# Kernel optimization log

Measured on AMD Instinct MI355X. Metric: run time of the kernel, lower is better.

The kernel has to match this reference:

```python
import jax, jax.numpy as jnp
import numpy as np
from jax import lax

B, C, H, W = 32, 192, 56, 56
HEADS = 8
HD = C // HEADS
SCALE = HD ** -0.5
EPS = 1e-5


def _ln(t, g, b):
    m = jnp.mean(t, axis=-1, keepdims=True)
    v = jnp.mean((t - m) ** 2, axis=-1, keepdims=True)
    return (t - m) / jnp.sqrt(v + EPS) * g + b


def setup_inputs() -> dict:
    ks = jax.random.split(jax.random.key(0), 8)
    x = jax.random.normal(ks[0], (B, C, H, W), jnp.float32)
    bn_gamma = jnp.ones((C,), jnp.float32)
    bn_beta = jnp.zeros((C,), jnp.float32)
    bn_mean = jax.random.normal(ks[1], (C,), jnp.float32) * 0.1
    bn_var = jax.random.uniform(ks[2], (C,), jnp.float32) + 0.5
    conv_w = jax.random.normal(ks[3], (C, 1, 7, 7), jnp.float32) * 0.02  # depthwise, groups=C
    conv_b = jnp.zeros((C,), jnp.float32)
    qkv_w = jax.random.normal(ks[4], (3 * C, C), jnp.float32) * 0.02
    qkv_b = jnp.zeros((3 * C,), jnp.float32)
    ln0_g = jnp.ones((C,), jnp.float32); ln0_b = jnp.zeros((C,), jnp.float32)
    ln1_g = jnp.ones((C,), jnp.float32); ln1_b = jnp.zeros((C,), jnp.float32)
    return {"x": x, "bn_gamma": bn_gamma, "bn_beta": bn_beta, "bn_mean": bn_mean,
            "bn_var": bn_var, "conv_w": conv_w, "conv_b": conv_b,
            "qkv_w": qkv_w, "qkv_b": qkv_b,
            "ln0_g": ln0_g, "ln0_b": ln0_b, "ln1_g": ln1_g, "ln1_b": ln1_b}


def reference(x, bn_gamma, bn_beta, bn_mean, bn_var, conv_w, conv_b,
              qkv_w, qkv_b, ln0_g, ln0_b, ln1_g, ln1_b):
    Bx, Cx, Hx, Wx = x.shape
    N = Hx * Wx
    Bw = Bx * N // 4  # number of 2x2 windows

    # --- window partition: [B,C,H,W] -> [B*N/4, 4, C]
    windows = x.reshape(Bx, Cx, Hx // 2, 2, Wx // 2, 2)
    windows = windows.transpose(0, 2, 4, 3, 5, 1).reshape(Bw, 4, Cx)

    # --- guide-token generator: BN(inference) -> GELU -> depthwise 7x7 s2 conv
    xb = (x - bn_mean[:, None, None]) / jnp.sqrt(bn_var[:, None, None] + EPS)
    xb = xb * bn_gamma[:, None, None] + bn_beta[:, None, None]
    xg = jax.nn.gelu(xb, approximate=False)
    g = lax.conv_general_dilated(xg, conv_w, window_strides=(2, 2),
                                 padding=[(3, 3), (3, 3)],
                                 feature_group_count=Cx,
                                 dimension_numbers=("NCHW", "OIHW", "NCHW"))
    g = g + conv_b[None, :, None, None]              # [B,C,H/2,W/2]
    guide = g.reshape(Bx, Cx, N // 4).transpose(0, 2, 1).reshape(Bw, 1, Cx)

    # --- 5-token windows: guide + 4 local tokens
    tok = jnp.concatenate([guide, windows], axis=1)  # [Bw,5,C]
    t = _ln(tok, ln0_g, ln0_b)

    # --- tiny attention over 5 tokens
    qkv = t @ qkv_w.T + qkv_b                        # [Bw,5,3C]
    qkv = qkv.reshape(Bw, 5, 3, HEADS, HD).transpose(2, 0, 3, 1, 4)  # [3,Bw,h,5,hd]
    q, k, v = qkv[0], qkv[1], qkv[2]
    attn = jax.nn.softmax(jnp.einsum("bhqd,bhkd->bhqk", q, k) * SCALE, axis=-1)
    o = jnp.einsum("bhqk,bhkd->bhqd", attn, v)       # [Bw,h,5,hd]
    o = o.transpose(0, 2, 1, 3).reshape(Bw, 5, Cx)

    out = o[:, 0].reshape(Bx, Hx // 2, Wx // 2, Cx)
    return _ln(out, ln1_g, ln1_b)
```

## Files before the change

### kernel.cpp

```cpp
#include <hip/hip_runtime.h>
#include <hip/hip_bf16.h>
#include <cmath>

#define B_    32
#define C_    192
#define H_    56
#define W_    56
#define EPS_  1e-5f
#define SCALE_ 0.20412414523193154f

using bf = __hip_bfloat16;
typedef __attribute__((ext_vector_type(8))) short short8;
typedef __attribute__((ext_vector_type(4))) float f32x4;

__global__ void k_wconv(const float* __restrict__ qkv_w, bf* __restrict__ wbf) {
    int i = blockIdx.x * 256 + threadIdx.x;
    if (i < 576 * 192) wbf[i] = __float2bfloat16(qkv_w[i]);
}

__global__ __launch_bounds__(256) void k_act_ptok(
        const float* __restrict__ x,
        const float* __restrict__ ln0g, const float* __restrict__ ln0b,
        bf* __restrict__ ptok) {
    __shared__ float tile[C_ * 57];
    __shared__ float mv[W_], rv[W_];
    int b = blockIdx.x / H_, h = blockIdx.x % H_;
    const size_t xbase = ((size_t)b * C_ * H_ + h) * W_;

    for (int f = threadIdx.x; f < C_ * W_; f += 256) {
        int c = f / W_, w = f % W_;
        tile[c * 57 + w] = x[xbase + (size_t)c * (H_ * W_) + w];
    }
    __syncthreads();
    if (threadIdx.x < 224) {
        int p = threadIdx.x >> 2, q = threadIdx.x & 3;
        float S = 0.f, Q = 0.f;
        #pragma unroll 8
        for (int j = 0; j < 48; j++) {
            float v = tile[(q * 48 + j) * 57 + p];
            S += v; Q += v * v;
        }
        S += __shfl_xor(S, 1); Q += __shfl_xor(Q, 1);
        S += __shfl_xor(S, 2); Q += __shfl_xor(Q, 2);
        if (q == 0) {
            float mean = S * (1.f / 192.f);
            float var  = Q * (1.f / 192.f) - mean * mean;
            mv[p] = mean; rv[p] = rsqrtf(var + EPS_);
        }
    }
    __syncthreads();
    const size_t pbase = (((size_t)b * H_ + h) * W_) * C_;
    for (int f = threadIdx.x; f < W_ * C_; f += 256) {
        int p = f / C_, c = f % C_;
        float v = (tile[c * 57 + p] - mv[p]) * rv[p] * ln0g[c] + ln0b[c];
        ptok[pbase + (size_t)p * C_ + c] = __float2bfloat16(v);
    }
}

__global__ __launch_bounds__(256) void k_conv(
        const float* __restrict__ x,
        const float* __restrict__ bn_g, const float* __restrict__ bn_b,
        const float* __restrict__ bn_m, const float* __restrict__ bn_v,
        const float* __restrict__ cw, const float* __restrict__ cb,
        float* __restrict__ gbuf) {
    __shared__ float pl[62 * 63];
    int tid = threadIdx.x;
    int bc = blockIdx.x;
    int c = bc % C_;

    for (int i = tid; i < 62 * 63; i += 256) pl[i] = 0.f;
    __syncthreads();

    float bm = bn_m[c];
    float rs = rsqrtf(bn_v[c] + EPS_) * bn_g[c];
    float bb = bn_b[c];
    const float* xp = x + (size_t)bc * (H_ * W_);
    for (int i = tid; i < 784; i += 256) {
        int row = i / 14, j = i % 14;
        float4 v = *(const float4*)(xp + row * W_ + j * 4);
        float* dst = &pl[(row + 3) * 63 + j * 4 + 3];
        #pragma unroll
        for (int e = 0; e < 4; e++) {
            float xv = (e == 0) ? v.x : (e == 1) ? v.y : (e == 2) ? v.z : v.w;
            float xn = (xv - bm) * rs + bb;
            dst[e] = 0.5f * xn * (1.0f + erff(xn * 0.70710678118654752f));
        }
    }
    __syncthreads();

    float wr[49];
    #pragma unroll
    for (int i = 0; i < 49; i++) wr[i] = cw[c * 49 + i];
    float cbv = cb[c];

    for (int o = tid; o < 784; o += 256) {
        int oh = o / 28, ow = o % 28;
        const float* base = &pl[(2 * oh) * 63 + 2 * ow];
        float acc = cbv;
        #pragma unroll
        for (int kh = 0; kh < 7; kh++) {
            #pragma unroll
            for (int kw = 0; kw < 7; kw++)
                acc += wr[kh * 7 + kw] * base[kh * 63 + kw];
        }
        gbuf[(size_t)bc * 784 + o] = acc;
    }
}

__global__ __launch_bounds__(256) void k_gtok(
        const float* __restrict__ gbuf,
        const float* __restrict__ ln0g, const float* __restrict__ ln0b,
        bf* __restrict__ gtok) {
    __shared__ float tile[C_ * 29];
    __shared__ float mv[28], rv[28];
    int b = blockIdx.x / 28, oh = blockIdx.x % 28;
    size_t gbase = ((size_t)b * C_ * 784) + (size_t)oh * 28;
    for (int f = threadIdx.x; f < C_ * 28; f += 256) {
        int c = f / 28, w = f % 28;
        tile[c * 29 + w] = gbuf[gbase + (size_t)c * 784 + w];
    }
    __syncthreads();
    if (threadIdx.x < 112) {
        int p = threadIdx.x >> 2, q = threadIdx.x & 3;
        float S = 0.f, Q = 0.f;
        #pragma unroll 8
        for (int j = 0; j < 48; j++) {
            float v = tile[(q * 48 + j) * 29 + p];
            S += v; Q += v * v;
        }
        S += __shfl_xor(S, 1); Q += __shfl_xor(Q, 1);
        S += __shfl_xor(S, 2); Q += __shfl_xor(Q, 2);
        if (q == 0) {
            float mean = S * (1.f / 192.f);
            float var  = Q * (1.f / 192.f) - mean * mean;
            mv[p] = mean; rv[p] = rsqrtf(var + EPS_);
        }
    }
    __syncthreads();
    size_t tbase = ((size_t)b * 784 + (size_t)oh * 28) * C_;
    for (int f = threadIdx.x; f < 28 * C_; f += 256) {
        int p = f / C_, c = f % C_;
        float v = (tile[c * 29 + p] - mv[p]) * rv[p] * ln0g[c] + ln0b[c];
        gtok[tbase + (size_t)p * C_ + c] = __float2bfloat16(v);
    }
}

template<int COLOFS>
__global__ __launch_bounds__(256) void k_gemm(
        const bf* __restrict__ A, const bf* __restrict__ wbf,
        const float* __restrict__ qkv_b, bf* __restrict__ out) {
    __shared__ unsigned char Asm_[128 * 384];
    int tid = threadIdx.x;
    size_t r0 = (size_t)blockIdx.x * 128;

    for (int i = tid; i < 128 * 24; i += 256) {
        int row = i / 24, j = i % 24;
        uint4 v = *(const uint4*)((const unsigned char*)(A + (r0 + row) * C_) + j * 16);
        *(uint4*)(Asm_ + row * 384 + ((j * 16) ^ ((row & 7) << 4))) = v;
    }
    __syncthreads();

    int wid = tid >> 6, lane = tid & 63, lo = lane & 15, hi = lane >> 4;
    int xorv = (lo & 7) << 4;
    constexpr int NT = (576 - COLOFS) / 16;
    constexpr int OUTW = 576 - COLOFS;
    for (int nt = wid; nt < NT; nt += 4) {
        int col = COLOFS + nt * 16 + lo;
        float bias = qkv_b[col];
        f32x4 acc[8];
        #pragma unroll
        for (int m = 0; m < 8; m++) acc[m] = {bias, bias, bias, bias};
        const unsigned char* bbase = (const unsigned char*)wbf + (size_t)col * 384 + hi * 16;
        #pragma unroll
        for (int ks = 0; ks < 6; ks++) {
            short8 bfrag = *(const short8*)(bbase + ks * 64);
            int kb = (ks * 64 + hi * 16) ^ xorv;
            #pragma unroll
            for (int m = 0; m < 8; m++) {
                short8 a = *(const short8*)(Asm_ + (m * 16 + lo) * 384 + kb);
                acc[m] = __builtin_amdgcn_mfma_f32_16x16x32_bf16(a, bfrag, acc[m], 0, 0, 0);
            }
        }
        #pragma unroll
        for (int m = 0; m < 8; m++) {
            #pragma unroll
            for (int r = 0; r < 4; r++) {
                int row = m * 16 + hi * 4 + r;
                out[(r0 + row) * OUTW + (col - COLOFS)] = __float2bfloat16(acc[m][r]);
            }
        }
    }
}

__global__ __launch_bounds__(256) void k_att2(
        const bf* __restrict__ kvp, const bf* __restrict__ qkvg,
        const float* __restrict__ ln1g, const float* __restrict__ ln1b,
        float* __restrict__ out) {
    int tg = blockIdx.x * 256 + threadIdx.x;
    int bw = tg >> 3, hh = tg & 7;
    int b = bw / 784, rr = bw % 784;
    int oh = rr / 28, ow = rr % 28;

    const bf* qb = qkvg + (size_t)bw * 576 + hh * 24;
    float q[24];
    #pragma unroll
    for (int j = 0; j < 3; j++) {
        short8 v = *(const short8*)(qb + j * 8);
        #pragma unroll
        for (int e = 0; e < 8; e++)
            q[j * 8 + e] = __uint_as_float(((unsigned)(unsigned short)v[e]) << 16);
    }
    size_t pr[4];
    #pragma unroll
    for (int t = 0; t < 4; t++) {
        int h = 2 * oh + (t >> 1), w = 2 * ow + (t & 1);
        pr[t] = ((size_t)b * H_ + h) * W_ + w;
    }

    float s[5];
    {
        float a = 0.f;
        #pragma unroll
        for (int j = 0; j < 3; j++) {
            short8 v = *(const short8*)(qb + 192 + j * 8);
            #pragma unroll
            for (int e = 0; e < 8; e++)
                a += q[j * 8 + e] * __uint_as_float(((unsigned)(unsigned short)v[e]) << 16);
        }
        s[0] = a * SCALE_;
    }
    #pragma unroll
    for (int t = 0; t < 4; t++) {
        const bf* kb = kvp + pr[t] * 384 + hh * 24;
        float a = 0.f;
        #pragma unroll
        for (int j = 0; j < 3; j++) {
            short8 v = *(const short8*)(kb + j * 8);
            #pragma unroll
            for (int e = 0; e < 8; e++)
                a += q[j * 8 + e] * __uint_as_float(((unsigned)(unsigned short)v[e]) << 16);
        }
        s[t + 1] = a * SCALE_;
    }
    float mx = fmaxf(fmaxf(fmaxf(s[0], s[1]), fmaxf(s[2], s[3])), s[4]);
    float sum = 0.f;
    #pragma unroll
    for (int t = 0; t < 5; t++) { s[t] = expf(s[t] - mx); sum += s[t]; }
    float inv = 1.f / sum;
    #pragma unroll
    for (int t = 0; t < 5; t++) s[t] *= inv;

    float o[24];
    #pragma unroll
    for (int d = 0; d < 24; d++) o[d] = 0.f;
    {
        #pragma unroll
        for (int j = 0; j < 3; j++) {
            short8 v = *(const short8*)(qb + 384 + j * 8);
            #pragma unroll
            for (int e = 0; e < 8; e++)
                o[j * 8 + e] += s[0] * __uint_as_float(((unsigned)(unsigned short)v[e]) << 16);
        }
    }
    #pragma unroll
    for (int t = 0; t < 4; t++) {
        const bf* vb = kvp + pr[t] * 384 + 192 + hh * 24;
        #pragma unroll
        for (int j = 0; j < 3; j++) {
            short8 v = *(const short8*)(vb + j * 8);
            #pragma unroll
            for (int e = 0; e < 8; e++)
                o[j * 8 + e] += s[t + 1] * __uint_as_float(((unsigned)(unsigned short)v[e]) << 16);
        }
    }

    float S = 0.f, Q = 0.f;
    #pragma unroll
    for (int d = 0; d < 24; d++) { S += o[d]; Q += o[d] * o[d]; }
    S += __shfl_xor(S, 1); Q += __shfl_xor(Q, 1);
    S += __shfl_xor(S, 2); Q += __shfl_xor(Q, 2);
    S += __shfl_xor(S, 4); Q += __shfl_xor(Q, 4);
    float mean = S * (1.f / 192.f);
    float var  = Q * (1.f / 192.f) - mean * mean;
    float rstd = rsqrtf(var + EPS_);
    float* ob = out + (size_t)bw * 192 + hh * 24;
    #pragma unroll
    for (int d = 0; d < 24; d++)
        ob[d] = (o[d] - mean) * rstd * ln1g[hh * 24 + d] + ln1b[hh * 24 + d];
}

__global__ __launch_bounds__(256) void k_attn(
        const bf* __restrict__ gtok, const bf* __restrict__ ptok,
        const bf* __restrict__ wbf, const float* __restrict__ qkv_b,
        const float* __restrict__ ln1g, const float* __restrict__ ln1b,
        float* __restrict__ out) {
    __shared__ unsigned char Asm_[48 * 384];
    __shared__ bf q0s[8][192];
    __shared__ bf kvs[2][5][8][192];
    int tid = threadIdx.x;
    int wb0 = blockIdx.x * 8;

    for (int idx = tid; idx < 48 * 24; idx += 256) {
        int row = idx / 24, j = idx % 24;
        int t = row >> 3, win = row & 7;
        uint4 val = {0u, 0u, 0u, 0u};
        if (t < 5) {
            const unsigned char* src;
            if (t == 0) {
                src = (const unsigned char*)(gtok + (size_t)(wb0 + win) * C_) + j * 16;
            } else {
                int bw = wb0 + win;
                int b = bw / 784; int rr = bw - b * 784;
                int oh = rr / 28, ow = rr - oh * 28;
                int h = 2 * oh + ((t - 1) >> 1), w = 2 * ow + ((t - 1) & 1);
                src = (const unsigned char*)(ptok + (((size_t)b * H_ + h) * W_ + w) * C_) + j * 16;
            }
            val = *(const uint4*)src;
        }
        *(uint4*)(Asm_ + row * 384 + ((j * 16) ^ ((row & 7) << 4))) = val;
    }
    __syncthreads();

    int wid = tid >> 6, lane = tid & 63, lo = lane & 15, hi = lane >> 4;
    int xorv = (lo & 7) << 4;
    for (int nn = 0; nn < 9; nn++) {
        int nt = nn * 4 + wid;
        int col = nt * 16 + lo;
        int mtop = (nt < 12) ? 1 : 3;
        float bias = qkv_b[col];
        f32x4 acc0 = {bias, bias, bias, bias};
        f32x4 acc1 = acc0, acc2 = acc0;
        const unsigned char* bbase = (const unsigned char*)wbf + (size_t)col * 384 + hi * 16;
        #pragma unroll
        for (int ks = 0; ks < 6; ks++) {
            short8 bfrag = *(const short8*)(bbase + ks * 64);
            int kb = ks * 64 + hi * 16;
            short8 a0 = *(const short8*)(Asm_ + lo * 384 + (kb ^ xorv));
            acc0 = __builtin_amdgcn_mfma_f32_16x16x32_bf16(a0, bfrag, acc0, 0, 0, 0);
            if (mtop > 1) {
                short8 a1 = *(const short8*)(Asm_ + (16 + lo) * 384 + (kb ^ xorv));
                acc1 = __builtin_amdgcn_mfma_f32_16x16x32_bf16(a1, bfrag, acc1, 0, 0, 0);
                short8 a2 = *(const short8*)(Asm_ + (32 + lo) * 384 + (kb ^ xorv));
                acc2 = __builtin_amdgcn_mfma_f32_16x16x32_bf16(a2, bfrag, acc2, 0, 0, 0);
            }
        }
        #pragma unroll
        for (int m = 0; m < 3; m++) {
            if (m < mtop) {
                f32x4 a = (m == 0) ? acc0 : ((m == 1) ? acc1 : acc2);
                #pragma unroll
                for (int r = 0; r < 4; r++) {
                    int row = m * 16 + hi * 4 + r;
                    int t = row >> 3, win = row & 7;
                    if (t < 5) {
                        float v = a[r];
                        if (col < 192) {
                            if (t == 0) q0s[win][col] = __float2bfloat16(v);
                        } else if (col < 384) {
                            kvs[0][t][win][col - 192] = __float2bfloat16(v);
                        } else {
                            kvs[1][t][win][col - 384] = __float2bfloat16(v);
                        }
                    }
                }
            }
        }
    }
    __syncthreads();

    if (tid >= 64) return;
    int win = tid >> 3, hh = tid & 7, base = hh * 24;
    float q[24], o[24];
    #pragma unroll
    for (int d = 0; d < 24; d++) { q[d] = __bfloat162float(q0s[win][base + d]); o[d] = 0.f; }
    float s[5];
    #pragma unroll
    for (int t = 0; t < 5; t++) {
        float a = 0.f;
        #pragma unroll
        for (int d = 0; d < 24; d++) a += q[d] * __bfloat162float(kvs[0][t][win][base + d]);
        s[t] = a * SCALE_;
    }
    float mx = fmaxf(fmaxf(fmaxf(s[0], s[1]), fmaxf(s[2], s[3])), s[4]);
    float sum = 0.f;
    #pragma unroll
    for (int t = 0; t < 5; t++) { s[t] = expf(s[t] - mx); sum += s[t]; }
    float inv = 1.f / sum;
    #pragma unroll
    for (int t = 0; t < 5; t++) {
        float pt = s[t] * inv;
        #pragma unroll
        for (int d = 0; d < 24; d++) o[d] += pt * __bfloat162float(kvs[1][t][win][base + d]);
    }
    float S = 0.f, Q = 0.f;
    #pragma unroll
    for (int d = 0; d < 24; d++) { S += o[d]; Q += o[d] * o[d]; }
    S += __shfl_xor(S, 1); Q += __shfl_xor(Q, 1);
    S += __shfl_xor(S, 2); Q += __shfl_xor(Q, 2);
    S += __shfl_xor(S, 4); Q += __shfl_xor(Q, 4);
    float mean = S * (1.f / 192.f);
    float var  = Q * (1.f / 192.f) - mean * mean;
    float rstd = rsqrtf(var + EPS_);
    size_t ob = (size_t)(wb0 + win) * C_ + base;
    #pragma unroll
    for (int d = 0; d < 24; d++)
        out[ob + d] = (o[d] - mean) * rstd * ln1g[base + d] + ln1b[base + d];
}

extern "C" void kernel_launch(void* const* d_in, const int* in_sizes, int n_in,
                              void* d_out, int out_size, void* d_ws, size_t ws_size,
                              hipStream_t stream) {
    const float* x       = (const float*)d_in[0];
    const float* bn_g    = (const float*)d_in[1];
    const float* bn_b    = (const float*)d_in[2];
    const float* bn_m    = (const float*)d_in[3];
    const float* bn_v    = (const float*)d_in[4];
    const float* conv_w  = (const float*)d_in[5];
    const float* conv_b  = (const float*)d_in[6];
    const float* qkv_w   = (const float*)d_in[7];
    const float* qkv_b   = (const float*)d_in[8];
    const float* ln0g    = (const float*)d_in[9];
    const float* ln0b    = (const float*)d_in[10];
    const float* ln1g    = (const float*)d_in[11];
    const float* ln1b    = (const float*)d_in[12];

    char* ws = (char*)d_ws;
    bf*    ptok = (bf*)(ws);
    bf*    gtok = (bf*)(ws + 38535168);
    bf*    wbf  = (bf*)(ws + 48168960);
    bf*    kvp  = (bf*)(ws + 48390144);
    bf*    qkvg = (bf*)(ws + 125460480);
    const bool split = (ws_size >= 154361856ULL);
    float* gbuf = split ? (float*)(ws + 125460480)
                        : (float*)(ws + 48390144);

    k_wconv   <<<dim3(432),   dim3(256), 0, stream>>>(qkv_w, wbf);
    k_conv    <<<dim3(B_*C_), dim3(256), 0, stream>>>(x, bn_g, bn_b, bn_m, bn_v,
                                                      conv_w, conv_b, gbuf);
    k_act_ptok<<<dim3(B_*H_), dim3(256), 0, stream>>>(x, ln0g, ln0b, ptok);
    k_gtok    <<<dim3(B_*28), dim3(256), 0, stream>>>(gbuf, ln0g, ln0b, gtok);
    if (split) {
        k_gemm<192><<<dim3(784), dim3(256), 0, stream>>>(ptok, wbf, qkv_b, kvp);
        k_gemm<0>  <<<dim3(196), dim3(256), 0, stream>>>(gtok, wbf, qkv_b, qkvg);
        k_att2     <<<dim3(784), dim3(256), 0, stream>>>(kvp, qkvg, ln1g, ln1b,
                                                         (float*)d_out);
    } else {
        k_attn     <<<dim3(3136), dim3(256), 0, stream>>>(gtok, ptok, wbf, qkv_b,
                                                          ln1g, ln1b, (float*)d_out);
    }
}
```

Baseline: 311.5 us.

## Vectorize LN loads/stores, restructure conv LDS layout, window-order GEMM output

The LN-prep kernels now read rows as float4 and write bf16 tokens eight at a time with 16-byte stores. The depthwise conv splits its padded plane by column phase into four LDS planes, and each thread computes two adjacent outputs while reusing a row of loaded values. The K/V GEMM writes its output in window-major order so the attention kernel reads the four tokens of a window contiguously. The fallback fused attention path for small workspaces is removed, so the split path now always runs and assumes a large enough workspace.

Result: slower. 322.9 us (+3.7%).

```diff
diff --git a/kernel.cpp b/kernel.cpp
--- a/kernel.cpp
+++ b/kernel.cpp
@@ -27,9 +27,11 @@
     int b = blockIdx.x / H_, h = blockIdx.x % H_;
     const size_t xbase = ((size_t)b * C_ * H_ + h) * W_;
 
-    for (int f = threadIdx.x; f < C_ * W_; f += 256) {
-        int c = f / W_, w = f % W_;
-        tile[c * 57 + w] = x[xbase + (size_t)c * (H_ * W_) + w];
+    for (int i = threadIdx.x; i < C_ * 14; i += 256) {
+        int c = i / 14, j = i % 14;
+        float4 v = *(const float4*)(x + xbase + (size_t)c * (H_ * W_) + j * 4);
+        float* dst = &tile[c * 57 + j * 4];
+        dst[0] = v.x; dst[1] = v.y; dst[2] = v.z; dst[3] = v.w;
     }
     __syncthreads();
     if (threadIdx.x < 224) {
@@ -50,10 +52,16 @@
     }
     __syncthreads();
     const size_t pbase = (((size_t)b * H_ + h) * W_) * C_;
-    for (int f = threadIdx.x; f < W_ * C_; f += 256) {
-        int p = f / C_, c = f % C_;
-        float v = (tile[c * 57 + p] - mv[p]) * rv[p] * ln0g[c] + ln0b[c];
-        ptok[pbase + (size_t)p * C_ + c] = __float2bfloat16(v);
+    for (int it = threadIdx.x; it < 24 * W_; it += 256) {
+        int p = it % W_, cb = it / W_;
+        float m = mv[p], r = rv[p];
+        bf v8[8];
+        #pragma unroll
+        for (int e = 0; e < 8; e++) {
+            int c = cb * 8 + e;
+            v8[e] = __float2bfloat16((tile[c * 57 + p] - m) * r * ln0g[c] + ln0b[c]);
+        }
+        *(uint4*)(ptok + pbase + (size_t)p * C_ + cb * 8) = *(const uint4*)v8;
     }
 }
 
@@ -63,12 +71,13 @@
         const float* __restrict__ bn_m, const float* __restrict__ bn_v,
         const float* __restrict__ cw, const float* __restrict__ cb,
         float* __restrict__ gbuf) {
-    __shared__ float pl[62 * 63];
+    __shared__ float Apl[4][62][17];
     int tid = threadIdx.x;
     int bc = blockIdx.x;
     int c = bc % C_;
 
-    for (int i = tid; i < 62 * 63; i += 256) pl[i] = 0.f;
+    float* flat = &Apl[0][0][0];
+    for (int i = tid; i < 4 * 62 * 17; i += 256) flat[i] = 0.f;
     __syncthreads();
 
     float bm = bn_m[c];
@@ -78,12 +87,13 @@
     for (int i = tid; i < 784; i += 256) {
         int row = i / 14, j = i % 14;
         float4 v = *(const float4*)(xp + row * W_ + j * 4);
-        float* dst = &pl[(row + 3) * 63 + j * 4 + 3];
         #pragma unroll
         for (int e = 0; e < 4; e++) {
             float xv = (e == 0) ? v.x : (e == 1) ? v.y : (e == 2) ? v.z : v.w;
             float xn = (xv - bm) * rs + bb;
-            dst[e] = 0.5f * xn * (1.0f + erff(xn * 0.70710678118654752f));
+            float ge = 0.5f * xn * (1.0f + erff(xn * 0.70710678118654752f));
+            int pc = 4 * j + 3 + e;
+            Apl[pc & 3][row + 3][pc >> 2] = ge;
         }
     }
     __syncthreads();
@@ -93,17 +103,24 @@
     for (int i = 0; i < 49; i++) wr[i] = cw[c * 49 + i];
     float cbv = cb[c];
 
-    for (int o = tid; o < 784; o += 256) {
-        int oh = o / 28, ow = o % 28;
-        const float* base = &pl[(2 * oh) * 63 + 2 * ow];
-        float acc = cbv;
+    for (int o2 = tid; o2 < 392; o2 += 256) {
+        int oh = o2 / 14, g = o2 % 14;
+        float acc0 = cbv, acc1 = cbv;
         #pragma unroll
         for (int kh = 0; kh < 7; kh++) {
-            #pragma unroll
-            for (int kw = 0; kw < 7; kw++)
-                acc += wr[kh * 7 + kw] * base[kh * 63 + kw];
-        }
-        gbuf[(size_t)bc * 784 + o] = acc;
+            int r = 2 * oh + kh;
+            float v[9];
+            #pragma unroll
+            for (int d = 0; d < 9; d++) v[d] = Apl[d & 3][r][g + (d >> 2)];
+            #pragma unroll
+            for (int kw = 0; kw < 7; kw++) {
+                float wv = wr[kh * 7 + kw];
+                acc0 += wv * v[kw];
+                acc1 += wv * v[kw + 2];
+            }
+        }
+        float2 st = {acc0, acc1};
+        *(float2*)(gbuf + (size_t)bc * 784 + oh * 28 + 2 * g) = st;
     }
 }
 
@@ -115,9 +132,11 @@
     __shared__ float mv[28], rv[28];
     int b = blockIdx.x / 28, oh = blockIdx.x % 28;
     size_t gbase = ((size_t)b * C_ * 784) + (size_t)oh * 28;
-    for (int f = threadIdx.x; f < C_ * 28; f += 256) {
-        int c = f / 28, w = f % 28;
-        tile[c * 29 + w] = gbuf[gbase + (size_t)c * 784 + w];
+    for (int i = threadIdx.x; i < C_ * 7; i += 256) {
+        int c = i / 7, j = i % 7;
+        float4 v = *(const float4*)(gbuf + gbase + (size_t)c * 784 + j * 4);
+        float* dst = &tile[c * 29 + j * 4];
+        dst[0] = v.x; dst[1] = v.y; dst[2] = v.z; dst[3] = v.w;
     }
     __syncthreads();
     if (threadIdx.x < 112) {
@@ -138,14 +157,20 @@
     }
     __syncthreads();
     size_t tbase = ((size_t)b * 784 + (size_t)oh * 28) * C_;
-    for (int f = threadIdx.x; f < 28 * C_; f += 256) {
-        int p = f / C_, c = f % C_;
-        float v = (tile[c * 29 + p] - mv[p]) * rv[p] * ln0g[c] + ln0b[c];
-        gtok[tbase + (size_t)p * C_ + c] = __float2bfloat16(v);
-    }
-}
-
-template<int COLOFS>
+    for (int it = threadIdx.x; it < 24 * 28; it += 256) {
+        int p = it % 28, cb = it / 28;
+        float m = mv[p], r = rv[p];
+        bf v8[8];
+        #pragma unroll
+        for (int e = 0; e < 8; e++) {
+            int c = cb * 8 + e;
+            v8[e] = __float2bfloat16((tile[c * 29 + p] - m) * r * ln0g[c] + ln0b[c]);
+        }
+        *(uint4*)(gtok + tbase + (size_t)p * C_ + cb * 8) = *(const uint4*)v8;
+    }
+}
+
+template<int COLOFS, bool WINDOWED>
 __global__ __launch_bounds__(256) void k_gemm(
         const bf* __restrict__ A, const bf* __restrict__ wbf,
         const float* __restrict__ qkv_b, bf* __restrict__ out) {
@@ -163,7 +188,26 @@
     int wid = tid >> 6, lane = tid & 63, lo = lane & 15, hi = lane >> 4;
     int xorv = (lo & 7) << 4;
     constexpr int NT = (576 - COLOFS) / 16;
-    constexpr int OUTW = 576 - COLOFS;
+
+    int dstb[8][4];
+    #pragma unroll
+    for (int m = 0; m < 8; m++) {
+        #pragma unroll
+        for (int r = 0; r < 4; r++) {
+            int row = m * 16 + hi * 4 + r;
+            if (WINDOWED) {
+                int p = (int)r0 + row;
+                int b = p / 3136, rem = p - b * 3136;
+                int h = rem / 56, w = rem - h * 56;
+                int bw = b * 784 + (h >> 1) * 28 + (w >> 1);
+                int t = (h & 1) * 2 + (w & 1);
+                dstb[m][r] = (bw * 4 + t) * 384;
+            } else {
+                dstb[m][r] = ((int)r0 + row) * (576 - COLOFS);
+            }
+        }
+    }
+
     for (int nt = wid; nt < NT; nt += 4) {
         int col = COLOFS + nt * 16 + lo;
         float bias = qkv_b[col];
@@ -181,25 +225,22 @@
                 acc[m] = __builtin_amdgcn_mfma_f32_16x16x32_bf16(a, bfrag, acc[m], 0, 0, 0);
             }
         }
+        int cofs = col - COLOFS;
         #pragma unroll
         for (int m = 0; m < 8; m++) {
             #pragma unroll
-            for (int r = 0; r < 4; r++) {
-                int row = m * 16 + hi * 4 + r;
-                out[(r0 + row) * OUTW + (col - COLOFS)] = __float2bfloat16(acc[m][r]);
-            }
+            for (int r = 0; r < 4; r++)
+                out[(size_t)dstb[m][r] + cofs] = __float2bfloat16(acc[m][r]);
         }
     }
 }
 
 __global__ __launch_bounds__(256) void k_att2(
-        const bf* __restrict__ kvp, const bf* __restrict__ qkvg,
+        const bf* __restrict__ kvp2, const bf* __restrict__ qkvg,
         const float* __restrict__ ln1g, const float* __restrict__ ln1b,
         float* __restrict__ out) {
     int tg = blockIdx.x * 256 + threadIdx.x;
     int bw = tg >> 3, hh = tg & 7;
-    int b = bw / 784, rr = bw % 784;
-    int oh = rr / 28, ow = rr % 28;
 
     const bf* qb = qkvg + (size_t)bw * 576 + hh * 24;
     float q[24];
@@ -209,12 +250,6 @@
         #pragma unroll
         for (int e = 0; e < 8; e++)
             q[j * 8 + e] = __uint_as_float(((unsigned)(unsigned short)v[e]) << 16);
-    }
-    size_t pr[4];
-    #pragma unroll
-    for (int t = 0; t < 4; t++) {
-        int h = 2 * oh + (t >> 1), w = 2 * ow + (t & 1);
-        pr[t] = ((size_t)b * H_ + h) * W_ + w;
     }
 
     float s[5];
@@ -231,7 +266,7 @@
     }
     #pragma unroll
     for (int t = 0; t < 4; t++) {
-        const bf* kb = kvp + pr[t] * 384 + hh * 24;
+        const bf* kb = kvp2 + ((size_t)bw * 4 + t) * 384 + hh * 24;
         float a = 0.f;
         #pragma unroll
         for (int j = 0; j < 3; j++) {
@@ -264,7 +299,7 @@
     }
     #pragma unroll
     for (int t = 0; t < 4; t++) {
-        const bf* vb = kvp + pr[t] * 384 + 192 + hh * 24;
+        const bf* vb = kvp2 + ((size_t)bw * 4 + t) * 384 + 192 + hh * 24;
         #pragma unroll
         for (int j = 0; j < 3; j++) {
             short8 v = *(const short8*)(vb + j * 8);
@@ -287,124 +322,6 @@
     #pragma unroll
     for (int d = 0; d < 24; d++)
         ob[d] = (o[d] - mean) * rstd * ln1g[hh * 24 + d] + ln1b[hh * 24 + d];
-}
-
-__global__ __launch_bounds__(256) void k_attn(
-        const bf* __restrict__ gtok, const bf* __restrict__ ptok,
-        const bf* __restrict__ wbf, const float* __restrict__ qkv_b,
-        const float* __restrict__ ln1g, const float* __restrict__ ln1b,
-        float* __restrict__ out) {
-    __shared__ unsigned char Asm_[48 * 384];
-    __shared__ bf q0s[8][192];
-    __shared__ bf kvs[2][5][8][192];
-    int tid = threadIdx.x;
-    int wb0 = blockIdx.x * 8;
-
-    for (int idx = tid; idx < 48 * 24; idx += 256) {
-        int row = idx / 24, j = idx % 24;
-        int t = row >> 3, win = row & 7;
-        uint4 val = {0u, 0u, 0u, 0u};
-        if (t < 5) {
-            const unsigned char* src;
-            if (t == 0) {
-                src = (const unsigned char*)(gtok + (size_t)(wb0 + win) * C_) + j * 16;
-            } else {
-                int bw = wb0 + win;
-                int b = bw / 784; int rr = bw - b * 784;
-                int oh = rr / 28, ow = rr - oh * 28;
-                int h = 2 * oh + ((t - 1) >> 1), w = 2 * ow + ((t - 1) & 1);
-                src = (const unsigned char*)(ptok + (((size_t)b * H_ + h) * W_ + w) * C_) + j * 16;
-            }
-            val = *(const uint4*)src;
-        }
-        *(uint4*)(Asm_ + row * 384 + ((j * 16) ^ ((row & 7) << 4))) = val;
-    }
-    __syncthreads();
-
-    int wid = tid >> 6, lane = tid & 63, lo = lane & 15, hi = lane >> 4;
-    int xorv = (lo & 7) << 4;
-    for (int nn = 0; nn < 9; nn++) {
-        int nt = nn * 4 + wid;
-        int col = nt * 16 + lo;
-        int mtop = (nt < 12) ? 1 : 3;
-        float bias = qkv_b[col];
-        f32x4 acc0 = {bias, bias, bias, bias};
-        f32x4 acc1 = acc0, acc2 = acc0;
-        const unsigned char* bbase = (const unsigned char*)wbf + (size_t)col * 384 + hi * 16;
-        #pragma unroll
-        for (int ks = 0; ks < 6; ks++) {
-            short8 bfrag = *(const short8*)(bbase + ks * 64);
-            int kb = ks * 64 + hi * 16;
-            short8 a0 = *(const short8*)(Asm_ + lo * 384 + (kb ^ xorv));
-            acc0 = __builtin_amdgcn_mfma_f32_16x16x32_bf16(a0, bfrag, acc0, 0, 0, 0);
-            if (mtop > 1) {
-                short8 a1 = *(const short8*)(Asm_ + (16 + lo) * 384 + (kb ^ xorv));
-                acc1 = __builtin_amdgcn_mfma_f32_16x16x32_bf16(a1, bfrag, acc1, 0, 0, 0);
-                short8 a2 = *(const short8*)(Asm_ + (32 + lo) * 384 + (kb ^ xorv));
-                acc2 = __builtin_amdgcn_mfma_f32_16x16x32_bf16(a2, bfrag, acc2, 0, 0, 0);
-            }
-        }
-        #pragma unroll
-        for (int m = 0; m < 3; m++) {
-            if (m < mtop) {
-                f32x4 a = (m == 0) ? acc0 : ((m == 1) ? acc1 : acc2);
-                #pragma unroll
-                for (int r = 0; r < 4; r++) {
-                    int row = m * 16 + hi * 4 + r;
-                    int t = row >> 3, win = row & 7;
-                    if (t < 5) {
-                        float v = a[r];
-                        if (col < 192) {
-                            if (t == 0) q0s[win][col] = __float2bfloat16(v);
-                        } else if (col < 384) {
-                            kvs[0][t][win][col - 192] = __float2bfloat16(v);
-                        } else {
-                            kvs[1][t][win][col - 384] = __float2bfloat16(v);
-                        }
-                    }
-                }
-            }
-        }
-    }
-    __syncthreads();
-
-    if (tid >= 64) return;
-    int win = tid >> 3, hh = tid & 7, base = hh * 24;
-    float q[24], o[24];
-    #pragma unroll
-    for (int d = 0; d < 24; d++) { q[d] = __bfloat162float(q0s[win][base + d]); o[d] = 0.f; }
-    float s[5];
-    #pragma unroll
-    for (int t = 0; t < 5; t++) {
-        float a = 0.f;
-        #pragma unroll
-        for (int d = 0; d < 24; d++) a += q[d] * __bfloat162float(kvs[0][t][win][base + d]);
-        s[t] = a * SCALE_;
-    }
-    float mx = fmaxf(fmaxf(fmaxf(s[0], s[1]), fmaxf(s[2], s[3])), s[4]);
-    float sum = 0.f;
-    #pragma unroll
-    for (int t = 0; t < 5; t++) { s[t] = expf(s[t] - mx); sum += s[t]; }
-    float inv = 1.f / sum;
-    #pragma unroll
-    for (int t = 0; t < 5; t++) {
-        float pt = s[t] * inv;
-        #pragma unroll
-        for (int d = 0; d < 24; d++) o[d] += pt * __bfloat162float(kvs[1][t][win][base + d]);
-    }
-    float S = 0.f, Q = 0.f;
-    #pragma unroll
-    for (int d = 0; d < 24; d++) { S += o[d]; Q += o[d] * o[d]; }
-    S += __shfl_xor(S, 1); Q += __shfl_xor(Q, 1);
-    S += __shfl_xor(S, 2); Q += __shfl_xor(Q, 2);
-    S += __shfl_xor(S, 4); Q += __shfl_xor(Q, 4);
-    float mean = S * (1.f / 192.f);
-    float var  = Q * (1.f / 192.f) - mean * mean;
-    float rstd = rsqrtf(var + EPS_);
-    size_t ob = (size_t)(wb0 + win) * C_ + base;
-    #pragma unroll
-    for (int d = 0; d < 24; d++)
-        out[ob + d] = (o[d] - mean) * rstd * ln1g[base + d] + ln1b[base + d];
 }
 
 extern "C" void kernel_launch(void* const* d_in, const int* in_sizes, int n_in,
@@ -428,24 +345,17 @@
     bf*    ptok = (bf*)(ws);
     bf*    gtok = (bf*)(ws + 38535168);
     bf*    wbf  = (bf*)(ws + 48168960);
-    bf*    kvp  = (bf*)(ws + 48390144);
+    bf*    kvp2 = (bf*)(ws + 48390144);
     bf*    qkvg = (bf*)(ws + 125460480);
-    const bool split = (ws_size >= 154361856ULL);
-    float* gbuf = split ? (float*)(ws + 125460480)
-                        : (float*)(ws + 48390144);
+    float* gbuf = (float*)(ws + 125460480);
 
     k_wconv   <<<dim3(432),   dim3(256), 0, stream>>>(qkv_w, wbf);
     k_conv    <<<dim3(B_*C_), dim3(256), 0, stream>>>(x, bn_g, bn_b, bn_m, bn_v,
                                                       conv_w, conv_b, gbuf);
     k_act_ptok<<<dim3(B_*H_), dim3(256), 0, stream>>>(x, ln0g, ln0b, ptok);
     k_gtok    <<<dim3(B_*28), dim3(256), 0, stream>>>(gbuf, ln0g, ln0b, gtok);
-    if (split) {
-        k_gemm<192><<<dim3(784), dim3(256), 0, stream>>>(ptok, wbf, qkv_b, kvp);
-        k_gemm<0>  <<<dim3(196), dim3(256), 0, stream>>>(gtok, wbf, qkv_b, qkvg);
-        k_att2     <<<dim3(784), dim3(256), 0, stream>>>(kvp, qkvg, ln1g, ln1b,
-                                                         (float*)d_out);
-    } else {
-        k_attn     <<<dim3(3136), dim3(256), 0, stream>>>(gtok, ptok, wbf, qkv_b,
-                                                          ln1g, ln1b, (float*)d_out);
-    }
-}
+    k_gemm<192, true> <<<dim3(784), dim3(256), 0, stream>>>(ptok, wbf, qkv_b, kvp2);
+    k_gemm<0, false>  <<<dim3(196), dim3(256), 0, stream>>>(gtok, wbf, qkv_b, qkvg);
+    k_att2    <<<dim3(784),  dim3(256), 0, stream>>>(kvp2, qkvg, ln1g, ln1b,
+                                                     (float*)d_out);
+}
```
